# Performance work log

Hardware: AMD Instinct MI355X
Metric: run time of the kernel (lower is better)

The kernel has to match this reference:

```python
import jax, jax.numpy as jnp
import numpy as np
import math

H, W = 128, 128  # output_dim = (H, W)
B = 4096


def setup_inputs() -> dict:
    key = jax.random.key(0)
    moments = jax.random.normal(key, (B, 6), dtype=jnp.float32)
    return {"moments": moments}


def reference(moments):
    sx, sy = float(W - 1), float(H - 1)
    # grid: [[x, y] for x in range(W) for y in range(H)] -> shape [W*H, 2]
    gx, gy = jnp.meshgrid(jnp.arange(W, dtype=jnp.float32),
                          jnp.arange(H, dtype=jnp.float32), indexing="ij")
    grid = jnp.stack([gx.reshape(-1), gy.reshape(-1)], axis=-1)  # [G, 2]

    scale = jnp.array([sx / 2.0, sy / 2.0], dtype=jnp.float32)
    mu = jnp.tanh(moments[:, :2]) * scale + scale  # [B, 2]

    t = jnp.tanh(moments[:, 2:5])
    lo = jnp.array([0.03, -0.999, 0.03], dtype=jnp.float32)
    hi = jnp.array([1.0, 0.999, 1.0], dtype=jnp.float32)
    t = jnp.clip(t, lo, hi)
    a = t[:, 0] * 3.0 * sx                                   # cov[0,0]
    b = t[:, 1] * jnp.sqrt(t[:, 0] * t[:, 2] * 9.0 * sx * sy)  # cov[0,1]
    c = t[:, 2] * 3.0 * sy                                   # cov[1,1]

    det = a * c - b * b  # closed-form 2x2 determinant
    it = 10.0 * jax.nn.sigmoid(moments[:, 5])
    norm = it / jnp.sqrt(det * (2.0 * math.pi) ** 2)  # [B]

    d = grid[None, :, :] - mu[:, None, :]  # [B, G, 2]
    dx, dy = d[..., 0], d[..., 1]
    # closed-form quadratic form d^T Sigma^{-1} d for 2x2 symmetric Sigma
    q = (c[:, None] * dx * dx - 2.0 * b[:, None] * dx * dy + a[:, None] * dy * dy) / det[:, None]
    img = norm[:, None] * jnp.exp(-0.5 * q)  # [B, G]
    # reshape (B, W, H) then transpose -> (B, H, W), matching tf reference
    return jnp.transpose(img.reshape(-1, W, H), (0, 2, 1))
```

## Files before the change

### kernel.cpp

```cpp
#include <hip/hip_runtime.h>
#include <math.h>

#define HH 128
#define WW 128

typedef float f32x4 __attribute__((ext_vector_type(4)));

__global__ __launch_bounds__(256) void MomentsToImage_kernel(
    const float* __restrict__ moments, float* __restrict__ out) {
    const int b = blockIdx.x;
    const float* m = moments + (size_t)b * 6;

    const float sx = (float)(WW - 1);
    const float sy = (float)(HH - 1);

    float m0 = m[0], m1 = m[1], m2 = m[2], m3 = m[3], m4 = m[4], m5 = m[5];

    float mux = tanhf(m0) * (sx * 0.5f) + (sx * 0.5f);
    float muy = tanhf(m1) * (sy * 0.5f) + (sy * 0.5f);

    float t0 = fminf(fmaxf(tanhf(m2), 0.03f),   1.0f);
    float t1 = fminf(fmaxf(tanhf(m3), -0.999f), 0.999f);
    float t2 = fminf(fmaxf(tanhf(m4), 0.03f),   1.0f);

    float a  = t0 * (3.0f * sx);
    float bb = t1 * sqrtf(t0 * t2 * (9.0f * sx * sy));
    float c  = t2 * (3.0f * sy);

    float det = a * c - bb * bb;
    float it  = 10.0f / (1.0f + __expf(-m5));
    float norm = it / (6.28318530717958647692f * sqrtf(det));

    float inv_det = 1.0f / det;
    const float L2E = 1.4426950408889634f;
    float P = (-0.5f * c * inv_det) * L2E;
    float Q = ( bb * inv_det)       * L2E;
    float R = (-0.5f * a * inv_det) * L2E;
    float n2 = __builtin_amdgcn_logf(norm);

    const int lane = threadIdx.x & 63;
    const int wid  = threadIdx.x >> 6;

    float d0 = (float)((lane & 31) << 2) - mux;
    float d1 = d0 + 1.0f;
    float d2 = d0 + 2.0f;
    float d3 = d0 + 3.0f;

    float A0 = P * d0 * d0 + n2, B0 = Q * d0;
    float A1 = P * d1 * d1 + n2, B1 = Q * d1;
    float A2 = P * d2 * d2 + n2, B2 = Q * d2;
    float A3 = P * d3 * d3 + n2, B3 = Q * d3;

    float dy = (float)((wid << 5) + (lane >> 5)) - muy;

    f32x4* out4 = (f32x4*)(out + (size_t)b * (HH * WW)) + (wid << 10) + lane;

    #pragma unroll
    for (int i = 0; i < 16; ++i) {
        float dy2 = dy * dy;
        float rb  = R * dy2;
        f32x4 o;
        o.x = __builtin_amdgcn_exp2f(fmaf(B0, dy, A0) + rb);
        o.y = __builtin_amdgcn_exp2f(fmaf(B1, dy, A1) + rb);
        o.z = __builtin_amdgcn_exp2f(fmaf(B2, dy, A2) + rb);
        o.w = __builtin_amdgcn_exp2f(fmaf(B3, dy, A3) + rb);
        __builtin_nontemporal_store(o, &out4[i * 64]);
        dy += 2.0f;
    }
}

extern "C" void kernel_launch(void* const* d_in, const int* in_sizes, int n_in,
                              void* d_out, int out_size, void* d_ws, size_t ws_size,
                              hipStream_t stream) {
    const float* moments = (const float*)d_in[0];
    float* out = (float*)d_out;
    int B = in_sizes[0] / 6;
    MomentsToImage_kernel<<<dim3(B), dim3(256), 0, stream>>>(moments, out);
}
```

Baseline: 266.6 us.

## Process eight images per block with prefetched moments and plain stores

Each block now loops over eight consecutive images instead of one, cutting the grid to B/8 blocks, and prefetches the next image's six moments while computing the current one. The nontemporal store hint is replaced with ordinary stores. The aim is to amortize block launch and scalar setup, hide the latency of the moments loads, and let writes go through the cache. In exchange each block does more serial work with fewer blocks in flight (512 blocks), and the launch assumes B is divisible by eight.

```diff
diff --git a/kernel.cpp b/kernel.cpp
--- a/kernel.cpp
+++ b/kernel.cpp
@@ -3,69 +3,87 @@
 
 #define HH 128
 #define WW 128
+#define IMGS 8
 
 typedef float f32x4 __attribute__((ext_vector_type(4)));
 
 __global__ __launch_bounds__(256) void MomentsToImage_kernel(
     const float* __restrict__ moments, float* __restrict__ out) {
-    const int b = blockIdx.x;
-    const float* m = moments + (size_t)b * 6;
+    const int b0 = blockIdx.x * IMGS;
 
     const float sx = (float)(WW - 1);
     const float sy = (float)(HH - 1);
 
-    float m0 = m[0], m1 = m[1], m2 = m[2], m3 = m[3], m4 = m[4], m5 = m[5];
-
-    float mux = tanhf(m0) * (sx * 0.5f) + (sx * 0.5f);
-    float muy = tanhf(m1) * (sy * 0.5f) + (sy * 0.5f);
-
-    float t0 = fminf(fmaxf(tanhf(m2), 0.03f),   1.0f);
-    float t1 = fminf(fmaxf(tanhf(m3), -0.999f), 0.999f);
-    float t2 = fminf(fmaxf(tanhf(m4), 0.03f),   1.0f);
-
-    float a  = t0 * (3.0f * sx);
-    float bb = t1 * sqrtf(t0 * t2 * (9.0f * sx * sy));
-    float c  = t2 * (3.0f * sy);
-
-    float det = a * c - bb * bb;
-    float it  = 10.0f / (1.0f + __expf(-m5));
-    float norm = it / (6.28318530717958647692f * sqrtf(det));
-
-    float inv_det = 1.0f / det;
-    const float L2E = 1.4426950408889634f;
-    float P = (-0.5f * c * inv_det) * L2E;
-    float Q = ( bb * inv_det)       * L2E;
-    float R = (-0.5f * a * inv_det) * L2E;
-    float n2 = __builtin_amdgcn_logf(norm);
-
     const int lane = threadIdx.x & 63;
     const int wid  = threadIdx.x >> 6;
 
-    float d0 = (float)((lane & 31) << 2) - mux;
-    float d1 = d0 + 1.0f;
-    float d2 = d0 + 2.0f;
-    float d3 = d0 + 3.0f;
+    const float x0  = (float)((lane & 31) << 2);
+    const float yy0 = (float)((wid << 5) + (lane >> 5));
 
-    float A0 = P * d0 * d0 + n2, B0 = Q * d0;
-    float A1 = P * d1 * d1 + n2, B1 = Q * d1;
-    float A2 = P * d2 * d2 + n2, B2 = Q * d2;
-    float A3 = P * d3 * d3 + n2, B3 = Q * d3;
+    const float* mc = moments + (size_t)b0 * 6;
+    float m0 = mc[0], m1 = mc[1], m2 = mc[2], m3 = mc[3], m4 = mc[4], m5 = mc[5];
 
-    float dy = (float)((wid << 5) + (lane >> 5)) - muy;
+    #pragma unroll 1
+    for (int k = 0; k < IMGS; ++k) {
+        const int b = b0 + k;
 
-    f32x4* out4 = (f32x4*)(out + (size_t)b * (HH * WW)) + (wid << 10) + lane;
+        float n0 = 0.f, n1 = 0.f, n2 = 0.f, n3 = 0.f, n4 = 0.f, n5 = 0.f;
+        if (k + 1 < IMGS) {
+            const float* mn = moments + (size_t)(b + 1) * 6;
+            n0 = mn[0]; n1 = mn[1]; n2 = mn[2];
+            n3 = mn[3]; n4 = mn[4]; n5 = mn[5];
+        }
 
-    #pragma unroll
-    for (int i = 0; i < 16; ++i) {
-        float dy2 = dy * dy;
-        float rb  = R * dy2;
-        f32x4 o;
-        o.x = __builtin_amdgcn_exp2f(fmaf(B0, dy, A0) + rb);
-        o.y = __builtin_amdgcn_exp2f(fmaf(B1, dy, A1) + rb);
-        o.z = __builtin_amdgcn_exp2f(fmaf(B2, dy, A2) + rb);
-        o.w = __builtin_amdgcn_exp2f(fmaf(B3, dy, A3) + rb);
-        __builtin_nontemporal_store(o, &out4[i * 64]);
-        dy += 2.0f;
+        float mux = tanhf(m0) * (sx * 0.5f) + (sx * 0.5f);
+        float muy = tanhf(m1) * (sy * 0.5f) + (sy * 0.5f);
+
+        float t0 = fminf(fmaxf(tanhf(m2), 0.03f),   1.0f);
+        float t1 = fminf(fmaxf(tanhf(m3), -0.999f), 0.999f);
+        float t2 = fminf(fmaxf(tanhf(m4), 0.03f),   1.0f);
+
+        float a  = t0 * (3.0f * sx);
+        float bb = t1 * sqrtf(t0 * t2 * (9.0f * sx * sy));
+        float c  = t2 * (3.0f * sy);
+
+        float det = a * c - bb * bb;
+        float it  = 10.0f / (1.0f + __expf(-m5));
+        float norm = it / (6.28318530717958647692f * sqrtf(det));
+
+        float inv_det = 1.0f / det;
+        const float L2E = 1.4426950408889634f;
+        float P = (-0.5f * c * inv_det) * L2E;
+        float Q = ( bb * inv_det)       * L2E;
+        float R = (-0.5f * a * inv_det) * L2E;
+        float n2l = __builtin_amdgcn_logf(norm);
+
+        float d0 = x0 - mux;
+        float d1 = d0 + 1.0f;
+        float d2 = d0 + 2.0f;
+        float d3 = d0 + 3.0f;
+
+        float A0 = P * d0 * d0 + n2l, B0 = Q * d0;
+        float A1 = P * d1 * d1 + n2l, B1 = Q * d1;
+        float A2 = P * d2 * d2 + n2l, B2 = Q * d2;
+        float A3 = P * d3 * d3 + n2l, B3 = Q * d3;
+
+        float dy = yy0 - muy;
+
+        f32x4* out4 = (f32x4*)(out + (size_t)b * (HH * WW)) + (wid << 10) + lane;
+
+        #pragma unroll
+        for (int i = 0; i < 16; ++i) {
+            float dy2 = dy * dy;
+            float rb  = R * dy2;
+            f32x4 o;
+            o.x = __builtin_amdgcn_exp2f(fmaf(B0, dy, A0) + rb);
+            o.y = __builtin_amdgcn_exp2f(fmaf(B1, dy, A1) + rb);
+            o.z = __builtin_amdgcn_exp2f(fmaf(B2, dy, A2) + rb);
+            o.w = __builtin_amdgcn_exp2f(fmaf(B3, dy, A3) + rb);
+            out4[i * 64] = o;
+            dy += 2.0f;
+        }
+
+        m0 = n0; m1 = n1; m2 = n2; m3 = n3; m4 = n4; m5 = n5;
     }
 }
 
@@ -75,5 +93,5 @@
     const float* moments = (const float*)d_in[0];
     float* out = (float*)d_out;
     int B = in_sizes[0] / 6;
-    MomentsToImage_kernel<<<dim3(B), dim3(256), 0, stream>>>(moments, out);
+    MomentsToImage_kernel<<<dim3(B / IMGS), dim3(256), 0, stream>>>(moments, out);
 }
```

Measured after the change: 251.3 us. 5.7% less time.
